# Kernel tuning notes

Hardware: AMD Instinct MI355X
Metric: run time of the kernel (lower is better)

## Reference

```python
import jax, jax.numpy as jnp
import numpy as np

N = 50000
E = 800000
IN_DIM = 128
HID = 64
OUT_DIM = 1
NEG_SLOPE = 0.2
EPS = 1e-16


def _glorot(key, shape):
    fan = shape[-1] + (shape[0] if len(shape) > 1 else shape[-1])
    lim = jnp.sqrt(6.0 / fan)
    return jax.random.uniform(key, shape, jnp.float32, -lim, lim)


def setup_inputs() -> dict:
    key = jax.random.key(0)
    ks = jax.random.split(key, 12)
    x = jax.random.normal(ks[0], (N, IN_DIM), jnp.float32)
    edge_index = jax.random.randint(ks[1], (2, E), 0, N, jnp.int64)
    # GATConv layer 1: in=128, out=64, heads=4, concat=True
    W1 = _glorot(ks[2], (4 * HID, IN_DIM))
    att_src1 = _glorot(ks[3], (4, HID))
    att_dst1 = _glorot(ks[4], (4, HID))
    b1 = jnp.zeros((4 * HID,), jnp.float32)
    # GATConv layer 2: in=256, out=64, heads=1, concat=True
    W2 = _glorot(ks[5], (HID, 4 * HID))
    att_src2 = _glorot(ks[6], (1, HID))
    att_dst2 = _glorot(ks[7], (1, HID))
    b2 = jnp.zeros((HID,), jnp.float32)
    # final Linear(hidden, 1)
    fc_w = _glorot(ks[8], (OUT_DIM, HID))
    fc_b = jnp.zeros((OUT_DIM,), jnp.float32)
    return {"x": x, "edge_index": edge_index, "W1": W1, "att_src1": att_src1,
            "att_dst1": att_dst1, "b1": b1, "W2": W2, "att_src2": att_src2,
            "att_dst2": att_dst2, "b2": b2, "fc_w": fc_w, "fc_b": fc_b}


def _gat_layer(x, src, dst, W, att_src, att_dst, bias, heads, out_ch):
    n = x.shape[0]
    xt = (x @ W.T).reshape(n, heads, out_ch)          # [N, H, C]
    a_src = jnp.sum(xt * att_src[None], axis=-1)      # [N, H]
    a_dst = jnp.sum(xt * att_dst[None], axis=-1)      # [N, H]
    e = a_src[src] + a_dst[dst]                       # [E', H]
    e = jnp.where(e > 0, e, NEG_SLOPE * e)            # LeakyReLU(0.2)
    # segment softmax over incoming edges of each dst node
    m = jax.ops.segment_max(e, dst, num_segments=n)
    e = jnp.exp(e - m[dst])
    s = jax.ops.segment_sum(e, dst, num_segments=n)
    alpha = e / (s[dst] + EPS)                        # [E', H]
    msg = xt[src] * alpha[:, :, None]                 # [E', H, C]
    out = jax.ops.segment_sum(msg, dst, num_segments=n)
    return out.reshape(n, heads * out_ch) + bias


def reference(x, edge_index, W1, att_src1, att_dst1, b1,
              W2, att_src2, att_dst2, b2, fc_w, fc_b):
    n = x.shape[0]
    # PyG GATConv default: add self-loops
    loops = jnp.arange(n, dtype=edge_index.dtype)
    src = jnp.concatenate([edge_index[0], loops])
    dst = jnp.concatenate([edge_index[1], loops])
    h = jax.nn.relu(_gat_layer(x, src, dst, W1, att_src1, att_dst1, b1, 4, HID))
    h = jax.nn.relu(_gat_layer(h, src, dst, W2, att_src2, att_dst2, b2, 1, HID))
    logits = h @ fc_w.T + fc_b                        # [N, 1]
    return jax.nn.sigmoid(logits).squeeze()
```

## Files before the change

### kernel.cpp

```cpp
#include <hip/hip_runtime.h>
#include <hip/hip_bf16.h>

#define NN 50000
#define EE 800000
#define ET (NN + EE)
#define SG ((NN + 255) / 256)
#define GB1 ((NN + 63) / 64)

typedef __attribute__((ext_vector_type(8))) short short8;
typedef __attribute__((ext_vector_type(4))) float f32x4;

__device__ __forceinline__ float bf2f(unsigned short u) {
    union { unsigned int i; float f; } v; v.i = ((unsigned int)u) << 16; return v.f;
}
__device__ __forceinline__ unsigned short f2bf(float f) {
    __hip_bfloat16 h = __float2bfloat16(f);
    return *reinterpret_cast<unsigned short*>(&h);
}
__device__ __forceinline__ float lrelu(float e) { return fmaxf(e, 0.2f * e); }


__global__ void k_hist(const int* __restrict__ dst, int* __restrict__ cnt) {
    int i = blockIdx.x * blockDim.x + threadIdx.x;
    if (i < EE) atomicAdd(&cnt[dst[i]], 1);
}

__global__ __launch_bounds__(256) void k_scan1(const int* __restrict__ cnt,
                                               int* __restrict__ tmp, int* __restrict__ bsum) {
    int b = blockIdx.x, t = threadIdx.x, i = b * 256 + t;
    int lane = t & 63, w = t >> 6;
    int v = (i < NN) ? cnt[i] : 0;
    int s = v;
    #pragma unroll
    for (int off = 1; off < 64; off <<= 1) {
        int u = __shfl_up(s, off);
        if (lane >= off) s += u;
    }
    __shared__ int ws[4];
    if (lane == 63) ws[w] = s;
    __syncthreads();
    if (t == 0) {
        int a = 0;
        #pragma unroll
        for (int k = 0; k < 4; k++) { int x = ws[k]; ws[k] = a; a += x; }
        bsum[b] = a;
    }
    __syncthreads();
    s += ws[w];
    if (i < NN) tmp[i] = s;
}

__global__ __launch_bounds__(256) void k_scan2(const int* __restrict__ bsum, int* __restrict__ boff) {
    int t = threadIdx.x, lane = t & 63, w = t >> 6;
    int v = (t < SG) ? bsum[t] : 0;
    int s = v;
    #pragma unroll
    for (int off = 1; off < 64; off <<= 1) {
        int u = __shfl_up(s, off);
        if (lane >= off) s += u;
    }
    __shared__ int ws[4];
    if (lane == 63) ws[w] = s;
    __syncthreads();
    if (t == 0) {
        int a = 0;
        #pragma unroll
        for (int k = 0; k < 4; k++) { int x = ws[k]; ws[k] = a; a += x; }
    }
    __syncthreads();
    s += ws[w];
    if (t < SG) boff[t] = s - v;
}

__global__ void k_scan3_prep(const int* __restrict__ tmp, const int* __restrict__ boff,
                             int* __restrict__ rowptr, int* __restrict__ writeptr,
                             int* __restrict__ csr) {
    int i = blockIdx.x * blockDim.x + threadIdx.x;
    if (i == 0) rowptr[0] = 0;
    if (i < NN) {
        int base = boff[i >> 8];
        int incl = tmp[i] + base + i + 1;
        rowptr[i + 1] = incl;
        int excl = ((i & 255) ? tmp[i - 1] + base : base) + i;
        csr[excl] = i;
        writeptr[i] = excl + 1;
    }
}

template<int K, int N, int NH, bool A_BF16>
__device__ __forceinline__ void gemm_body(
    int bid, const void* __restrict__ Aptr, const float* __restrict__ W,
    const float* __restrict__ atts, const float* __restrict__ attd,
    unsigned short* __restrict__ C, float* __restrict__ as_, float* __restrict__ ad_,
    int M)
{
    constexpr int KU  = K / 8;
    constexpr int KUH = KU / 2;
    constexpr int KC  = K / 32;
    constexpr int NW  = N / 4;
    constexpr int NI  = NW / 16;
    constexpr int ABYTES = 64 * KU * 16;
    constexpr int BBYTES = N * KUH * 16;
    constexpr int SMEM = ABYTES + BBYTES + (NH == 1 ? 2048 : 0);
    __shared__ char smem[SMEM];
    char* Ash = smem;
    char* Bsh = smem + ABYTES;
    unsigned short* Csh = (unsigned short*)smem;
    float* scsh = (float*)(smem + ABYTES + BBYTES);

    int t = threadIdx.x;
    int lane = t & 63, w = t >> 6;
    int colL = lane & 15, quad = lane >> 4;
    int m0 = bid * 64;

    {
        constexpr int CNT = 64 * KU / 256;
        #pragma unroll
        for (int i = 0; i < CNT; i++) {
            int v = t + 256 * i;
            int m = v / KU, u = v % KU;
            int gr = m0 + m; if (gr >= M) gr = M - 1;
            short8 val;
            if (A_BF16) {
                val = *(const short8*)((const unsigned short*)Aptr + (size_t)gr * K + u * 8);
            } else {
                const float* Af = (const float*)Aptr;
                float4 lo = *(const float4*)(Af + (size_t)gr * K + u * 8);
                float4 hi = *(const float4*)(Af + (size_t)gr * K + u * 8 + 4);
                val[0] = (short)f2bf(lo.x); val[1] = (short)f2bf(lo.y);
                val[2] = (short)f2bf(lo.z); val[3] = (short)f2bf(lo.w);
                val[4] = (short)f2bf(hi.x); val[5] = (short)f2bf(hi.y);
                val[6] = (short)f2bf(hi.z); val[7] = (short)f2bf(hi.w);
            }
            *(short8*)(Ash + ((size_t)m * KU + (u ^ (m & 7))) * 16) = val;
        }
    }

    f32x4 acc[4][NI];
    #pragma unroll
    for (int mi = 0; mi < 4; mi++)
        #pragma unroll
        for (int ni = 0; ni < NI; ni++) acc[mi][ni] = (f32x4){0.f, 0.f, 0.f, 0.f};

    #pragma unroll
    for (int kh = 0; kh < 2; kh++) {
        __syncthreads();
        {
            constexpr int CNT = N * KUH / 256;
            #pragma unroll
            for (int i = 0; i < CNT; i++) {
                int v = t + 256 * i;
                int n = v / KUH, uu = v % KUH;
                int u = kh * KUH + uu;
                float4 lo = *(const float4*)(W + (size_t)n * K + u * 8);
                float4 hi = *(const float4*)(W + (size_t)n * K + u * 8 + 4);
                short8 val;
                val[0] = (short)f2bf(lo.x); val[1] = (short)f2bf(lo.y);
                val[2] = (short)f2bf(lo.z); val[3] = (short)f2bf(lo.w);
                val[4] = (short)f2bf(hi.x); val[5] = (short)f2bf(hi.y);
                val[6] = (short)f2bf(hi.z); val[7] = (short)f2bf(hi.w);
                *(short8*)(Bsh + ((size_t)n * KUH + (uu ^ (n & 7))) * 16) = val;
            }
        }
        __syncthreads();
        #pragma unroll
        for (int kcl = 0; kcl < KC / 2; kcl++) {
            int uA = (kh * (KC / 2) + kcl) * 4 + quad;
            int uB = kcl * 4 + quad;
            short8 bfr[NI];
            #pragma unroll
            for (int ni = 0; ni < NI; ni++) {
                int n = w * NW + ni * 16 + colL;
                bfr[ni] = *(const short8*)(Bsh + ((size_t)n * KUH + (uB ^ (n & 7))) * 16);
            }
            #pragma unroll
            for (int mi = 0; mi < 4; mi++) {
                int m = mi * 16 + colL;
                short8 af = *(const short8*)(Ash + ((size_t)m * KU + (uA ^ (m & 7))) * 16);
                #pragma unroll
                for (int ni = 0; ni < NI; ni++)
                    acc[mi][ni] = __builtin_amdgcn_mfma_f32_16x16x32_bf16(af, bfr[ni], acc[mi][ni], 0, 0, 0);
            }
        }
    }
    __syncthreads();

    float asv[NI], adv[NI];
    #pragma unroll
    for (int ni = 0; ni < NI; ni++) {
        int na = (NH == 4) ? (w * 64 + ni * 16 + colL) : (w * 16 + colL);
        asv[ni] = atts[na];
        adv[ni] = attd[na];
    }
    #pragma unroll
    for (int mi = 0; mi < 4; mi++) {
        float ps[4] = {0.f, 0.f, 0.f, 0.f}, pd[4] = {0.f, 0.f, 0.f, 0.f};
        #pragma unroll
        for (int ni = 0; ni < NI; ni++)
            #pragma unroll
            for (int r = 0; r < 4; r++) {
                ps[r] += acc[mi][ni][r] * asv[ni];
                pd[r] += acc[mi][ni][r] * adv[ni];
            }
        #pragma unroll
        for (int off = 1; off < 16; off <<= 1)
            #pragma unroll
            for (int r = 0; r < 4; r++) {
                ps[r] += __shfl_xor(ps[r], off);
                pd[r] += __shfl_xor(pd[r], off);
            }
        if (colL == 0) {
            #pragma unroll
            for (int r = 0; r < 4; r++) {
                int rloc = mi * 16 + quad * 4 + r;
                if (NH == 4) {
                    int row = m0 + rloc;
                    if (row < M) {
                        as_[(size_t)row * 4 + w] = ps[r];
                        ad_[(size_t)row * 4 + w] = pd[r];
                    }
                } else {
                    scsh[(w * 64 + rloc) * 2 + 0] = ps[r];
                    scsh[(w * 64 + rloc) * 2 + 1] = pd[r];
                }
            }
        }
    }

    #pragma unroll
    for (int mi = 0; mi < 4; mi++)
        #pragma unroll
        for (int ni = 0; ni < NI; ni++)
            #pragma unroll
            for (int r = 0; r < 4; r++)
                Csh[(size_t)(mi * 16 + quad * 4 + r) * (N + 8) + w * NW + ni * 16 + colL] =
                    f2bf(acc[mi][ni][r]);
    __syncthreads();

    {
        constexpr int CNT = 64 * (N / 8) / 256;
        #pragma unroll
        for (int i = 0; i < CNT; i++) {
            int v = t + 256 * i;
            int m = v / (N / 8), u = v % (N / 8);
            int row = m0 + m;
            if (row < M)
                *(short8*)(C + (size_t)row * N + u * 8) =
                    *(const short8*)(Csh + (size_t)m * (N + 8) + u * 8);
        }
    }
    if (NH == 1 && t < 64) {
        int row = m0 + t;
        if (row < M) {
            float s = 0.f, d = 0.f;
            #pragma unroll
            for (int ww = 0; ww < 4; ww++) {
                s += scsh[(ww * 64 + t) * 2 + 0];
                d += scsh[(ww * 64 + t) * 2 + 1];
            }
            as_[row] = s;
            ad_[row] = d;
        }
    }
}

__global__ __launch_bounds__(256) void k_gemm1_scatter(
    const void* __restrict__ Aptr, const float* __restrict__ W,
    const float* __restrict__ atts, const float* __restrict__ attd,
    unsigned short* __restrict__ C, float* __restrict__ as_, float* __restrict__ ad_,
    int M,
    const int* __restrict__ src, const int* __restrict__ dst,
    int* __restrict__ writeptr, int* __restrict__ csr)
{
    int bid = blockIdx.x;
    int g = bid / 5, r = bid % 5;
    if (r == 0 && g < GB1) {
        gemm_body<128, 256, 4, false>(g, Aptr, W, atts, attd, C, as_, ad_, M);
    } else {
        int ng = (r == 0) ? g : g + 1;
        if (ng > GB1) ng = GB1;
        int sb = bid - ng;
        int i = sb * 256 + threadIdx.x;
        if (i < EE) {
            int pos = atomicAdd(&writeptr[dst[i]], 1);
            csr[pos] = src[i];
        }
    }
}

__global__ __launch_bounds__(256) void k_l1_gemm2(
    const unsigned short* __restrict__ xt1, const float* __restrict__ as1,
    const float* __restrict__ ad1, const int* __restrict__ rowptr,
    const int* __restrict__ csr, const float* __restrict__ b1,
    const float* __restrict__ W2, const float* __restrict__ atts2,
    const float* __restrict__ attd2,
    unsigned short* __restrict__ xt2, float* __restrict__ as2, float* __restrict__ ad2)
{
    __shared__ char smem[64 * 32 * 16 + 2048];
    char* Ash = smem;
    float* scsh = (float*)(smem + 64 * 32 * 16);
    unsigned short* Csh = (unsigned short*)smem;

    int t = threadIdx.x;
    int lane = t & 63, w = t >> 6;
    int half = lane >> 5, c = lane & 31, h = c >> 3;
    const char* xb = (const char*)xt1;
    const char* ab = (const char*)as1;
    unsigned co = (unsigned)(c << 4);
    unsigned ho = (unsigned)(h << 2);
    int m0 = blockIdx.x * 64;

    #pragma unroll 1
    for (int i = 0; i < 16; i++) {
        int m = w * 16 + i;
        int n = m0 + m;
        float acc[8] = {0.f, 0.f, 0.f, 0.f, 0.f, 0.f, 0.f, 0.f};
        float esum = 0.f;
        if (n < NN) {
            int beg = rowptr[n], deg = rowptr[n + 1] - beg;
            float adh = ad1[(n << 2) + h];
            int j = 0;
            if (deg >= 8) {
                int p = beg + half * 4;
                int s0 = csr[p], s1 = csr[p + 1], s2 = csr[p + 2], s3 = csr[p + 3];
                float a0 = *(const float*)(ab + ((unsigned)(s0 << 4) + ho));
                float a1 = *(const float*)(ab + ((unsigned)(s1 << 4) + ho));
                float a2 = *(const float*)(ab + ((unsigned)(s2 << 4) + ho));
                float a3 = *(const float*)(ab + ((unsigned)(s3 << 4) + ho));
                short8 r0 = *(const short8*)(xb + ((unsigned)(s0 << 9) + co));
                short8 r1 = *(const short8*)(xb + ((unsigned)(s1 << 9) + co));
                short8 r2 = *(const short8*)(xb + ((unsigned)(s2 << 9) + co));
                short8 r3 = *(const short8*)(xb + ((unsigned)(s3 << 9) + co));
                for (; j + 16 <= deg; j += 8) {
                    int p2 = beg + j + 8 + half * 4;
                    int u0 = csr[p2], u1 = csr[p2 + 1], u2 = csr[p2 + 2], u3 = csr[p2 + 3];
                    float f0 = *(const float*)(ab + ((unsigned)(u0 << 4) + ho));
                    float f1 = *(const float*)(ab + ((unsigned)(u1 << 4) + ho));
                    float f2 = *(const float*)(ab + ((unsigned)(u2 << 4) + ho));
                    float f3 = *(const float*)(ab + ((unsigned)(u3 << 4) + ho));
                    short8 q0 = *(const short8*)(xb + ((unsigned)(u0 << 9) + co));
                    short8 q1 = *(const short8*)(xb + ((unsigned)(u1 << 9) + co));
                    short8 q2 = *(const short8*)(xb + ((unsigned)(u2 << 9) + co));
                    short8 q3 = *(const short8*)(xb + ((unsigned)(u3 << 9) + co));
                    float e0 = __expf(lrelu(a0 + adh));
                    float e1 = __expf(lrelu(a1 + adh));
                    float e2 = __expf(lrelu(a2 + adh));
                    float e3 = __expf(lrelu(a3 + adh));
                    esum += (e0 + e1) + (e2 + e3);
                    #pragma unroll
                    for (int k = 0; k < 8; k++)
                        acc[k] += (bf2f((unsigned short)r0[k]) * e0 + bf2f((unsigned short)r1[k]) * e1)
                                + (bf2f((unsigned short)r2[k]) * e2 + bf2f((unsigned short)r3[k]) * e3);
                    a0 = f0; a1 = f1; a2 = f2; a3 = f3;
                    r0 = q0; r1 = q1; r2 = q2; r3 = q3;
                }
                {
                    float e0 = __expf(lrelu(a0 + adh));
                    float e1 = __expf(lrelu(a1 + adh));
                    float e2 = __expf(lrelu(a2 + adh));
                    float e3 = __expf(lrelu(a3 + adh));
                    esum += (e0 + e1) + (e2 + e3);
                    #pragma unroll
                    for (int k = 0; k < 8; k++)
                        acc[k] += (bf2f((unsigned short)r0[k]) * e0 + bf2f((unsigned short)r1[k]) * e1)
                                + (bf2f((unsigned short)r2[k]) * e2 + bf2f((unsigned short)r3[k]) * e3);
                    j += 8;
                }
            }
            if (j + 4 <= deg) {
                int p = beg + j + half * 2;
                int s0 = csr[p], s1 = csr[p + 1];
                float a0 = *(const float*)(ab + ((unsigned)(s0 << 4) + ho));
                float a1 = *(const float*)(ab + ((unsigned)(s1 << 4) + ho));
                short8 r0 = *(const short8*)(xb + ((unsigned)(s0 << 9) + co));
                short8 r1 = *(const short8*)(xb + ((unsigned)(s1 << 9) + co));
                float e0 = __expf(lrelu(a0 + adh));
                float e1 = __expf(lrelu(a1 + adh));
                esum += e0 + e1;
                #pragma unroll
                for (int k = 0; k < 8; k++)
                    acc[k] += bf2f((unsigned short)r0[k]) * e0 + bf2f((unsigned short)r1[k]) * e1;
                j += 4;
            }
            for (; j < deg; j += 2) {
                int jj = j + half;
                if (jj < deg) {
                    int s = csr[beg + jj];
                    float a0 = *(const float*)(ab + ((unsigned)(s << 4) + ho));
                    short8 r = *(const short8*)(xb + ((unsigned)(s << 9) + co));
                    float e = __expf(lrelu(a0 + adh));
                    esum += e;
                    #pragma unroll
                    for (int k = 0; k < 8; k++) acc[k] += bf2f((unsigned short)r[k]) * e;
                }
            }
        }
        #pragma unroll
        for (int k = 0; k < 8; k++) acc[k] += __shfl_xor(acc[k], 32);
        esum += __shfl_xor(esum, 32);
        if (half == 0) {
            short8 o;
            if (n < NN) {
                float rs = 1.f / (esum + 1e-16f);
                float4 bl = *(const float4*)(b1 + c * 8);
                float4 bh = *(const float4*)(b1 + c * 8 + 4);
                float bb[8] = {bl.x, bl.y, bl.z, bl.w, bh.x, bh.y, bh.z, bh.w};
                #pragma unroll
                for (int k = 0; k < 8; k++)
                    o[k] = (short)f2bf(fmaxf(acc[k] * rs + bb[k], 0.f));
            } else {
                #pragma unroll
                for (int k = 0; k < 8; k++) o[k] = 0;
            }
            *(short8*)(Ash + (((unsigned)(m * 32 + (c ^ (m & 7)))) << 4)) = o;
        }
    }

    int colL = lane & 15, quad = lane >> 4;
    short8 bf[8];
    {
        int nrow = w * 16 + colL;
        const float* wp = W2 + nrow * 256;
        #pragma unroll
        for (int kc = 0; kc < 8; kc++) {
            const float* p = wp + (kc * 4 + quad) * 8;
            float4 lo = *(const float4*)p;
            float4 hi = *(const float4*)(p + 4);
            short8 v;
            v[0] = (short)f2bf(lo.x); v[1] = (short)f2bf(lo.y);
            v[2] = (short)f2bf(lo.z); v[3] = (short)f2bf(lo.w);
            v[4] = (short)f2bf(hi.x); v[5] = (short)f2bf(hi.y);
            v[6] = (short)f2bf(hi.z); v[7] = (short)f2bf(hi.w);
            bf[kc] = v;
        }
    }
    __syncthreads();

    f32x4 acc2[4];
    #pragma unroll
    for (int mi = 0; mi < 4; mi++) acc2[mi] = (f32x4){0.f, 0.f, 0.f, 0.f};
    #pragma unroll
    for (int kc = 0; kc < 8; kc++) {
        int uA = kc * 4 + quad;
        #pragma unroll
        for (int mi = 0; mi < 4; mi++) {
            int mm = mi * 16 + colL;
            short8 af = *(const short8*)(Ash + (((unsigned)(mm * 32 + (uA ^ (mm & 7)))) << 4));
            acc2[mi] = __builtin_amdgcn_mfma_f32_16x16x32_bf16(af, bf[kc], acc2[mi], 0, 0, 0);
        }
    }

    {
        float asv = atts2[w * 16 + colL];
        float adv = attd2[w * 16 + colL];
        #pragma unroll
        for (int mi = 0; mi < 4; mi++) {
            float ps[4], pd[4];
            #pragma unroll
            for (int r = 0; r < 4; r++) { ps[r] = acc2[mi][r] * asv; pd[r] = acc2[mi][r] * adv; }
            #pragma unroll
            for (int off = 1; off < 16; off <<= 1)
                #pragma unroll
                for (int r = 0; r < 4; r++) {
                    ps[r] += __shfl_xor(ps[r], off);
                    pd[r] += __shfl_xor(pd[r], off);
                }
            if (colL == 0) {
                #pragma unroll
                for (int r = 0; r < 4; r++) {
                    int rloc = mi * 16 + quad * 4 + r;
                    scsh[(w * 64 + rloc) * 2 + 0] = ps[r];
                    scsh[(w * 64 + rloc) * 2 + 1] = pd[r];
                }
            }
        }
    }
    __syncthreads();

    #pragma unroll
    for (int mi = 0; mi < 4; mi++)
        #pragma unroll
        for (int r = 0; r < 4; r++)
            Csh[(size_t)(mi * 16 + quad * 4 + r) * 72 + w * 16 + colL] = f2bf(acc2[mi][r]);
    if (t < 64) {
        int row = m0 + t;
        if (row < NN) {
            float s = 0.f, d = 0.f;
            #pragma unroll
            for (int ww = 0; ww < 4; ww++) {
                s += scsh[(ww * 64 + t) * 2 + 0];
                d += scsh[(ww * 64 + t) * 2 + 1];
            }
            as2[row] = s;
            ad2[row] = d;
        }
    }
    __syncthreads();
    #pragma unroll
    for (int i2 = 0; i2 < 2; i2++) {
        int v = t + 256 * i2;
        int mm = v >> 3, u = v & 7;
        int row = m0 + mm;
        if (row < NN)
            *(short8*)(xt2 + (size_t)row * 64 + u * 8) =
                *(const short8*)(Csh + (size_t)mm * 72 + u * 8);
    }
}

__global__ __launch_bounds__(256) void k_l2_agg(
    const unsigned short* __restrict__ xt2, const float* __restrict__ as2,
    const float* __restrict__ ad2, const int* __restrict__ rowptr,
    const int* __restrict__ csr, const float* __restrict__ b2,
    const float* __restrict__ fcw, const float* __restrict__ fcb,
    float* __restrict__ out)
{
    int t = threadIdx.x;
    int lane = t & 63, w = t >> 6;
    int n = blockIdx.x * 4 + w;
    int beg = rowptr[n], deg = rowptr[n + 1] - beg;
    int q = lane >> 4, c = lane & 15;
    float adv = ad2[n];
    const char* xb = (const char*)xt2;
    unsigned co = (unsigned)(c << 3);

    float acc[4] = {0.f, 0.f, 0.f, 0.f};
    float esum = 0.f;
    int j = 0;
    if (deg >= 8) {
        int p = beg + q * 2;
        int s0 = csr[p], s1 = csr[p + 1];
        float a0 = as2[s0], a1 = as2[s1];
        uint2 r0 = *(const uint2*)(xb + ((unsigned)(s0 << 7) + co));
        uint2 r1 = *(const uint2*)(xb + ((unsigned)(s1 << 7) + co));
        for (; j + 16 <= deg; j += 8) {
            int p2 = beg + j + 8 + q * 2;
            int u0 = csr[p2], u1 = csr[p2 + 1];
            float f0 = as2[u0], f1 = as2[u1];
            uint2 q0 = *(const uint2*)(xb + ((unsigned)(u0 << 7) + co));
            uint2 q1 = *(const uint2*)(xb + ((unsigned)(u1 << 7) + co));
            float e0 = __expf(lrelu(a0 + adv));
            float e1 = __expf(lrelu(a1 + adv));
            esum += e0 + e1;
            acc[0] += bf2f((unsigned short)(r0.x & 0xffff)) * e0 + bf2f((unsigned short)(r1.x & 0xffff)) * e1;
            acc[1] += bf2f((unsigned short)(r0.x >> 16)) * e0 + bf2f((unsigned short)(r1.x >> 16)) * e1;
            acc[2] += bf2f((unsigned short)(r0.y & 0xffff)) * e0 + bf2f((unsigned short)(r1.y & 0xffff)) * e1;
            acc[3] += bf2f((unsigned short)(r0.y >> 16)) * e0 + bf2f((unsigned short)(r1.y >> 16)) * e1;
            a0 = f0; a1 = f1; r0 = q0; r1 = q1;
        }
        {
            float e0 = __expf(lrelu(a0 + adv));
            float e1 = __expf(lrelu(a1 + adv));
            esum += e0 + e1;
            acc[0] += bf2f((unsigned short)(r0.x & 0xffff)) * e0 + bf2f((unsigned short)(r1.x & 0xffff)) * e1;
            acc[1] += bf2f((unsigned short)(r0.x >> 16)) * e0 + bf2f((unsigned short)(r1.x >> 16)) * e1;
            acc[2] += bf2f((unsigned short)(r0.y & 0xffff)) * e0 + bf2f((unsigned short)(r1.y & 0xffff)) * e1;
            acc[3] += bf2f((unsigned short)(r0.y >> 16)) * e0 + bf2f((unsigned short)(r1.y >> 16)) * e1;
            j += 8;
        }
    }
    for (; j < deg; j += 4) {
        int jj = j + q;
        if (jj < deg) {
            int s = csr[beg + jj];
            float a0 = as2[s];
            uint2 r = *(const uint2*)(xb + ((unsigned)(s << 7) + co));
            float e = __expf(lrelu(a0 + adv));
            esum += e;
            acc[0] += bf2f((unsigned short)(r.x & 0xffff)) * e;
            acc[1] += bf2f((unsigned short)(r.x >> 16)) * e;
            acc[2] += bf2f((unsigned short)(r.y & 0xffff)) * e;
            acc[3] += bf2f((unsigned short)(r.y >> 16)) * e;
        }
    }
    #pragma unroll
    for (int k = 0; k < 4; k++) {
        acc[k] += __shfl_xor(acc[k], 16);
        acc[k] += __shfl_xor(acc[k], 32);
    }
    esum += __shfl_xor(esum, 16);
    esum += __shfl_xor(esum, 32);
    float rs = 1.f / (esum + 1e-16f);
    float4 bv = *(const float4*)(b2 + c * 4);
    float4 fv = *(const float4*)(fcw + c * 4);
    float z = fmaxf(acc[0] * rs + bv.x, 0.f) * fv.x
            + fmaxf(acc[1] * rs + bv.y, 0.f) * fv.y
            + fmaxf(acc[2] * rs + bv.z, 0.f) * fv.z
            + fmaxf(acc[3] * rs + bv.w, 0.f) * fv.w;
    #pragma unroll
    for (int off = 8; off; off >>= 1) z += __shfl_xor(z, off);
    if (lane == 0) out[n] = 1.f / (1.f + __expf(-(z + fcb[0])));
}


extern "C" void kernel_launch(void* const* d_in, const int* in_sizes, int n_in,
                              void* d_out, int out_size, void* d_ws, size_t ws_size,
                              hipStream_t stream) {
    const float* x    = (const float*)d_in[0];
    const int*   ei   = (const int*)d_in[1];
    const float* W1   = (const float*)d_in[2];
    const float* as1w = (const float*)d_in[3];
    const float* ad1w = (const float*)d_in[4];
    const float* b1   = (const float*)d_in[5];
    const float* W2   = (const float*)d_in[6];
    const float* as2w = (const float*)d_in[7];
    const float* ad2w = (const float*)d_in[8];
    const float* b2   = (const float*)d_in[9];
    const float* fcw  = (const float*)d_in[10];
    const float* fcb  = (const float*)d_in[11];
    float* out = (float*)d_out;

    const int* src = ei;
    const int* dst = ei + EE;

    char* base = (char*)d_ws;
    size_t off = 0;
    auto alloc = [&](size_t bytes) -> void* {
        void* p = base + off;
        off = (off + bytes + 255) & ~(size_t)255;
        return p;
    };
    int*   rowptr   = (int*)alloc((NN + 1) * sizeof(int));
    int*   cnt      = (int*)alloc(NN * sizeof(int));
    int*   tmp      = (int*)alloc(NN * sizeof(int));
    int*   bsum     = (int*)alloc(SG * sizeof(int));
    int*   boff     = (int*)alloc(SG * sizeof(int));
    int*   writeptr = (int*)alloc(NN * sizeof(int));
    int*   csr      = (int*)alloc(ET * sizeof(int));
    unsigned short* xt1 = (unsigned short*)alloc((size_t)NN * 256 * sizeof(unsigned short));
    unsigned short* xt2 = (unsigned short*)alloc((size_t)NN * 64 * sizeof(unsigned short));
    float* as1      = (float*)alloc(NN * 4 * sizeof(float));
    float* ad1      = (float*)alloc(NN * 4 * sizeof(float));
    float* as2      = (float*)alloc(NN * sizeof(float));
    float* ad2      = (float*)alloc(NN * sizeof(float));

    hipMemsetAsync(cnt, 0, NN * sizeof(int), stream);
    k_hist<<<(EE + 255) / 256, 256, 0, stream>>>(dst, cnt);
    k_scan1<<<SG, 256, 0, stream>>>(cnt, tmp, bsum);
    k_scan2<<<1, 256, 0, stream>>>(bsum, boff);
    k_scan3_prep<<<SG, 256, 0, stream>>>(tmp, boff, rowptr, writeptr, csr);

    int fused_blocks = GB1 + (EE + 255) / 256;
    k_gemm1_scatter<<<fused_blocks, 256, 0, stream>>>(
        x, W1, as1w, ad1w, xt1, as1, ad1, NN, src, dst, writeptr, csr);

    k_l1_gemm2<<<GB1, 256, 0, stream>>>(
        xt1, as1, ad1, rowptr, csr, b1, W2, as2w, ad2w, xt2, as2, ad2);

    k_l2_agg<<<(NN + 3) / 4, 256, 0, stream>>>(xt2, as2, ad2, rowptr, csr, b2, fcw, fcb, out);
}
```

Baseline: 281.6 us.

## Halve layer-1 aggregation block size and pre-convert W2 to bf16 once

The fused layer-1 aggregation plus GEMM2 kernel now handles 32 nodes per block instead of 64, which doubles the grid to about 1563 blocks and halves the per-block LDS and MFMA tile. The goal is better load balance and more blocks in flight for the latency-bound gather phase. W2 is converted to bf16 once inside the histogram kernel's first 16 blocks, so each block loads ready bf16 weights instead of converting fp32 on the fly. In exchange, every block repeats the W2 fragment load and the block-level synchronisation overhead, now amortised over half as many rows.

```diff
diff --git a/kernel.cpp b/kernel.cpp
--- a/kernel.cpp
+++ b/kernel.cpp
@@ -6,8 +6,11 @@
 #define ET (NN + EE)
 #define SG ((NN + 255) / 256)
 #define GB1 ((NN + 63) / 64)
+#define NB 32
+#define GB2 ((NN + NB - 1) / NB)
 
 typedef __attribute__((ext_vector_type(8))) short short8;
+typedef __attribute__((ext_vector_type(4))) short short4b;
 typedef __attribute__((ext_vector_type(4))) float f32x4;
 
 __device__ __forceinline__ float bf2f(unsigned short u) {
@@ -20,8 +23,18 @@
 __device__ __forceinline__ float lrelu(float e) { return fmaxf(e, 0.2f * e); }
 
 
-__global__ void k_hist(const int* __restrict__ dst, int* __restrict__ cnt) {
-    int i = blockIdx.x * blockDim.x + threadIdx.x;
+__global__ void k_hist(const int* __restrict__ dst, int* __restrict__ cnt,
+                       const float* __restrict__ W2, unsigned short* __restrict__ w2b) {
+    int t = threadIdx.x;
+    if (blockIdx.x < 16) {
+        int j = blockIdx.x * 256 + t;
+        float4 v = *(const float4*)(W2 + j * 4);
+        short4b o;
+        o[0] = (short)f2bf(v.x); o[1] = (short)f2bf(v.y);
+        o[2] = (short)f2bf(v.z); o[3] = (short)f2bf(v.w);
+        *(short4b*)(w2b + j * 4) = o;
+    }
+    int i = blockIdx.x * blockDim.x + t;
     if (i < EE) atomicAdd(&cnt[dst[i]], 1);
 }
 
@@ -292,13 +305,13 @@
     const unsigned short* __restrict__ xt1, const float* __restrict__ as1,
     const float* __restrict__ ad1, const int* __restrict__ rowptr,
     const int* __restrict__ csr, const float* __restrict__ b1,
-    const float* __restrict__ W2, const float* __restrict__ atts2,
+    const unsigned short* __restrict__ w2b, const float* __restrict__ atts2,
     const float* __restrict__ attd2,
     unsigned short* __restrict__ xt2, float* __restrict__ as2, float* __restrict__ ad2)
 {
-    __shared__ char smem[64 * 32 * 16 + 2048];
+    __shared__ char smem[NB * 32 * 16 + 1024];
     char* Ash = smem;
-    float* scsh = (float*)(smem + 64 * 32 * 16);
+    float* scsh = (float*)(smem + NB * 32 * 16);
     unsigned short* Csh = (unsigned short*)smem;
 
     int t = threadIdx.x;
@@ -308,11 +321,11 @@
     const char* ab = (const char*)as1;
     unsigned co = (unsigned)(c << 4);
     unsigned ho = (unsigned)(h << 2);
-    int m0 = blockIdx.x * 64;
+    int m0 = blockIdx.x * NB;
 
     #pragma unroll 1
-    for (int i = 0; i < 16; i++) {
-        int m = w * 16 + i;
+    for (int i = 0; i < 8; i++) {
+        int m = w * 8 + i;
         int n = m0 + m;
         float acc[8] = {0.f, 0.f, 0.f, 0.f, 0.f, 0.f, 0.f, 0.f};
         float esum = 0.f;
@@ -419,31 +432,21 @@
     int colL = lane & 15, quad = lane >> 4;
     short8 bf[8];
     {
-        int nrow = w * 16 + colL;
-        const float* wp = W2 + nrow * 256;
-        #pragma unroll
-        for (int kc = 0; kc < 8; kc++) {
-            const float* p = wp + (kc * 4 + quad) * 8;
-            float4 lo = *(const float4*)p;
-            float4 hi = *(const float4*)(p + 4);
-            short8 v;
-            v[0] = (short)f2bf(lo.x); v[1] = (short)f2bf(lo.y);
-            v[2] = (short)f2bf(lo.z); v[3] = (short)f2bf(lo.w);
-            v[4] = (short)f2bf(hi.x); v[5] = (short)f2bf(hi.y);
-            v[6] = (short)f2bf(hi.z); v[7] = (short)f2bf(hi.w);
-            bf[kc] = v;
-        }
-    }
-    __syncthreads();
-
-    f32x4 acc2[4];
-    #pragma unroll
-    for (int mi = 0; mi < 4; mi++) acc2[mi] = (f32x4){0.f, 0.f, 0.f, 0.f};
+        const unsigned short* wp = w2b + (w * 16 + colL) * 256;
+        #pragma unroll
+        for (int kc = 0; kc < 8; kc++)
+            bf[kc] = *(const short8*)(wp + (kc * 4 + quad) * 8);
+    }
+    __syncthreads();
+
+    f32x4 acc2[2];
+    #pragma unroll
+    for (int mi = 0; mi < 2; mi++) acc2[mi] = (f32x4){0.f, 0.f, 0.f, 0.f};
     #pragma unroll
     for (int kc = 0; kc < 8; kc++) {
         int uA = kc * 4 + quad;
         #pragma unroll
-        for (int mi = 0; mi < 4; mi++) {
+        for (int mi = 0; mi < 2; mi++) {
             int mm = mi * 16 + colL;
             short8 af = *(const short8*)(Ash + (((unsigned)(mm * 32 + (uA ^ (mm & 7)))) << 4));
             acc2[mi] = __builtin_amdgcn_mfma_f32_16x16x32_bf16(af, bf[kc], acc2[mi], 0, 0, 0);
@@ -454,7 +457,7 @@
         float asv = atts2[w * 16 + colL];
         float adv = attd2[w * 16 + colL];
         #pragma unroll
-        for (int mi = 0; mi < 4; mi++) {
+        for (int mi = 0; mi < 2; mi++) {
             float ps[4], pd[4];
             #pragma unroll
             for (int r = 0; r < 4; r++) { ps[r] = acc2[mi][r] * asv; pd[r] = acc2[mi][r] * adv; }
@@ -469,8 +472,8 @@
                 #pragma unroll
                 for (int r = 0; r < 4; r++) {
                     int rloc = mi * 16 + quad * 4 + r;
-                    scsh[(w * 64 + rloc) * 2 + 0] = ps[r];
-                    scsh[(w * 64 + rloc) * 2 + 1] = pd[r];
+                    scsh[(w * NB + rloc) * 2 + 0] = ps[r];
+                    scsh[(w * NB + rloc) * 2 + 1] = pd[r];
                 }
             }
         }
@@ -478,28 +481,26 @@
     __syncthreads();
 
     #pragma unroll
-    for (int mi = 0; mi < 4; mi++)
+    for (int mi = 0; mi < 2; mi++)
         #pragma unroll
         for (int r = 0; r < 4; r++)
             Csh[(size_t)(mi * 16 + quad * 4 + r) * 72 + w * 16 + colL] = f2bf(acc2[mi][r]);
-    if (t < 64) {
+    if (t < NB) {
         int row = m0 + t;
         if (row < NN) {
             float s = 0.f, d = 0.f;
             #pragma unroll
             for (int ww = 0; ww < 4; ww++) {
-                s += scsh[(ww * 64 + t) * 2 + 0];
-                d += scsh[(ww * 64 + t) * 2 + 1];
+                s += scsh[(ww * NB + t) * 2 + 0];
+                d += scsh[(ww * NB + t) * 2 + 1];
             }
             as2[row] = s;
             ad2[row] = d;
         }
     }
     __syncthreads();
-    #pragma unroll
-    for (int i2 = 0; i2 < 2; i2++) {
-        int v = t + 256 * i2;
-        int mm = v >> 3, u = v & 7;
+    {
+        int mm = t >> 3, u = t & 7;
         int row = m0 + mm;
         if (row < NN)
             *(short8*)(xt2 + (size_t)row * 64 + u * 8) =
@@ -628,13 +629,14 @@
     int*   csr      = (int*)alloc(ET * sizeof(int));
     unsigned short* xt1 = (unsigned short*)alloc((size_t)NN * 256 * sizeof(unsigned short));
     unsigned short* xt2 = (unsigned short*)alloc((size_t)NN * 64 * sizeof(unsigned short));
+    unsigned short* w2b = (unsigned short*)alloc(64 * 256 * sizeof(unsigned short));
     float* as1      = (float*)alloc(NN * 4 * sizeof(float));
     float* ad1      = (float*)alloc(NN * 4 * sizeof(float));
     float* as2      = (float*)alloc(NN * sizeof(float));
     float* ad2      = (float*)alloc(NN * sizeof(float));
 
     hipMemsetAsync(cnt, 0, NN * sizeof(int), stream);
-    k_hist<<<(EE + 255) / 256, 256, 0, stream>>>(dst, cnt);
+    k_hist<<<(EE + 255) / 256, 256, 0, stream>>>(dst, cnt, W2, w2b);
     k_scan1<<<SG, 256, 0, stream>>>(cnt, tmp, bsum);
     k_scan2<<<1, 256, 0, stream>>>(bsum, boff);
     k_scan3_prep<<<SG, 256, 0, stream>>>(tmp, boff, rowptr, writeptr, csr);
@@ -643,8 +645,8 @@
     k_gemm1_scatter<<<fused_blocks, 256, 0, stream>>>(
         x, W1, as1w, ad1w, xt1, as1, ad1, NN, src, dst, writeptr, csr);
 
-    k_l1_gemm2<<<GB1, 256, 0, stream>>>(
-        xt1, as1, ad1, rowptr, csr, b1, W2, as2w, ad2w, xt2, as2, ad2);
+    k_l1_gemm2<<<GB2, 256, 0, stream>>>(
+        xt1, as1, ad1, rowptr, csr, b1, w2b, as2w, ad2w, xt2, as2, ad2);
 
     k_l2_agg<<<(NN + 3) / 4, 256, 0, stream>>>(xt2, as2, ad2, rowptr, csr, b2, fcw, fcb, out);
 }
```

After: 280.0 us. About the same (-0.5%).
